# Performance work log

Measured on AMD Instinct MI355X. Metric: run time of the kernel, lower is better.

## Reference

```python
import jax, jax.numpy as jnp
import numpy as np

B, K, N, E, T = 4096, 64, 100000, 128, 3


def setup_inputs() -> dict:
    key = jax.random.key(0)
    ks = jax.random.split(key, 16)
    f = lambda i, shape: jax.random.normal(ks[i], shape, dtype=jnp.float32) * 0.05
    return dict(
        nodes=jax.random.randint(ks[0], (B,), 0, N),
        neigh_idx=jax.random.randint(ks[1], (T, B, K), 0, N),
        node_emb=f(2, (N, E)),
        node_prof=f(3, (N, E)),
        neigh_emb=f(4, (T, N, E)),
        neigh_prof=f(5, (T, N, E)),
        W_f=f(6, (2 * E, E)), b_f=jnp.zeros((E,), jnp.float32),
        Wa1=f(7, (2 * E, E)), ba1=jnp.zeros((E,), jnp.float32),
        Wa2=f(8, (E, E)), ba2=jnp.zeros((E,), jnp.float32),
        Wa3=f(9, (E, 1)), ba3=jnp.zeros((1,), jnp.float32),
        W1=f(10, (E, E)), b1=jnp.zeros((E,), jnp.float32),
        W2=f(11, (E, E)), b2=jnp.zeros((E,), jnp.float32),
        Wc=f(12, (2 * E, E)), bc=jnp.zeros((E,), jnp.float32),
        Wt=f(13, (T * E, T)),
    )


def reference(nodes, neigh_idx, node_emb, node_prof, neigh_emb, neigh_prof,
              W_f, b_f, Wa1, ba1, Wa2, ba2, Wa3, ba3,
              W1, b1, W2, b2, Wc, bc, Wt):
    # fusion(emb, profile) = relu(Linear(concat(emb, profile)))
    fuse = lambda e, p: jax.nn.relu(jnp.concatenate([e, p], -1) @ W_f + b_f)

    nodes_fusion = fuse(node_emb[nodes], node_prof[nodes])            # [B,E]

    per_type = []
    for t in range(T):                                                 # small fixed loop over types
        idx = neigh_idx[t]                                             # [B,K]
        nf = fuse(neigh_emb[t][idx], neigh_prof[t][idx])               # [B,K,E]
        # attention MLP over (neighbor, node) pairs -> softmax over K neighbors
        x = jnp.concatenate(
            [nf, jnp.broadcast_to(nodes_fusion[:, None, :], nf.shape)], -1)  # [B,K,2E]
        h = jax.nn.relu(x @ Wa1 + ba1)
        h = jax.nn.relu(h @ Wa2 + ba2)
        att = jax.nn.softmax((h @ Wa3 + ba3).squeeze(-1), axis=1)      # [B,K]
        agg = jnp.einsum('bke,bk->be', nf, att)                        # weighted neighbor sum
        per_type.append(jax.nn.relu(agg @ W1 + b1))                    # linear_1 + relu

    type_agg = jnp.concatenate(per_type, axis=1)                       # [B,T*E]
    att_t = jax.nn.softmax(type_agg @ Wt, axis=1)                      # [B,T]
    final = jnp.einsum('bte,bt->be', type_agg.reshape(B, T, E), att_t)
    final = jax.nn.relu(final @ W2 + b2)                               # linear_2 + relu
    out = jax.nn.relu(jnp.concatenate([nodes_fusion, final], 1) @ Wc + bc)
    return out, att_t[:, :, None]
```

## Files before the change

kernel.cpp:

```cpp
#include <hip/hip_runtime.h>
#include <hip/hip_bf16.h>

#define B_ 4096
#define K_ 64
#define N_ 100000
#define E_ 128
#define T_ 3

typedef __bf16 bf16x8 __attribute__((ext_vector_type(8)));
typedef float  f32x4  __attribute__((ext_vector_type(4)));

static __device__ __forceinline__ bf16x8 cvt8r(f32x4 u, f32x4 v) {
    bf16x8 o;
    o[0] = (__bf16)u[0]; o[1] = (__bf16)u[1]; o[2] = (__bf16)u[2]; o[3] = (__bf16)u[3];
    o[4] = (__bf16)v[0]; o[5] = (__bf16)v[1]; o[6] = (__bf16)v[2]; o[7] = (__bf16)v[3];
    return o;
}

typedef const __attribute__((address_space(1))) void GAS;
typedef __attribute__((address_space(3))) void LAS;
static __device__ __forceinline__ void gload16(const void* g, void* l) {
    __builtin_amdgcn_global_load_lds((GAS*)g, (LAS*)l, 16, 0, 0);
}

#define MFMA16(a, b, c) __builtin_amdgcn_mfma_f32_16x16x32_bf16((a), (b), (c), 0, 0, 0)

__global__ __launch_bounds__(256)
void k_prep(const float* __restrict__ W_f, const float* __restrict__ Wa1,
            const float* __restrict__ Wa2, const float* __restrict__ W1,
            __bf16* __restrict__ WtF, __bf16* __restrict__ Wa1t,
            __bf16* __restrict__ Wa2t, __bf16* __restrict__ W1t) {
    const int n = blockIdx.x;
    const int k = threadIdx.x;
    if (blockIdx.y == 0) {
        WtF[n * 256 + k] = (__bf16)W_f[k * 128 + n];
    } else if (blockIdx.y == 1) {
        if (k < 128) Wa1t[n * 128 + k] = (__bf16)Wa1[k * 128 + n];
    } else if (blockIdx.y == 2) {
        if (k < 128) Wa2t[n * 128 + k] = (__bf16)Wa2[k * 128 + n];
    } else {
        if (k < 128) W1t[n * 128 + k] = (__bf16)W1[k * 128 + n];
    }
}

__global__ __launch_bounds__(128)
void k_node_fusion(const int* __restrict__ nodes,
                   const float* __restrict__ node_emb,
                   const float* __restrict__ node_prof,
                   const float* __restrict__ W_f, const float* __restrict__ b_f,
                   __bf16* __restrict__ nodes_fusion) {
    __shared__ float x[256];
    const int b = blockIdx.x;
    const int e = threadIdx.x;
    const int nd = nodes[b];
    x[e]       = node_emb[(size_t)nd * E_ + e];
    x[128 + e] = node_prof[(size_t)nd * E_ + e];
    __syncthreads();
    float acc = b_f[e];
#pragma unroll 8
    for (int i = 0; i < 256; ++i) acc = fmaf(x[i], W_f[i * E_ + e], acc);
    nodes_fusion[(size_t)b * E_ + e] = (__bf16)fmaxf(acc, 0.f);
}

__global__ __launch_bounds__(128)
void k_node_pre(const __bf16* __restrict__ nodes_fusion,
                const float* __restrict__ Wa1, const float* __restrict__ ba1,
                float* __restrict__ node_pre) {
    __shared__ float x[128];
    const int b = blockIdx.x;
    const int c = threadIdx.x;
    x[c] = (float)nodes_fusion[(size_t)b * E_ + c];
    __syncthreads();
    float acc = ba1[c];
#pragma unroll 8
    for (int i = 0; i < 128; ++i) acc = fmaf(x[i], Wa1[(128 + i) * E_ + c], acc);
    node_pre[(size_t)b * E_ + c] = acc;
}

#define NF_GRID 1024
#define NF_TPT (N_ / 16)
#define NF_NJOB (NF_TPT * T_)

__global__ __launch_bounds__(256, 4)
void k_nf(const float* __restrict__ neigh_emb,
          const float* __restrict__ neigh_prof,
          const __bf16* __restrict__ WtF, const float* __restrict__ b_f,
          __bf16* __restrict__ NFt) {
    __shared__ __align__(16) float  Xf[2][16 * 256];
    __shared__ __align__(16) __bf16 NFl[16 * 128];

    const int tid  = threadIdx.x;
    const int wid  = tid >> 6, lane = tid & 63;
    const int lr   = lane & 15, lk = lane >> 4;

    bf16x8 wf[16];
#pragma unroll
    for (int ks = 0; ks < 8; ++ks)
#pragma unroll
        for (int n = 0; n < 2; ++n)
            wf[ks * 2 + n] = *(const bf16x8*)&WtF[
                (size_t)(wid * 32 + n * 16 + lr) * 256 + ks * 32 + lk * 8];
    const float bb0 = b_f[wid * 32 + lr];
    const float bb1 = b_f[wid * 32 + 16 + lr];

    auto stage = [&](int j, int buf) {
        const int t    = j / NF_TPT;
        const int base = (j - t * NF_TPT) * 16;
        const float* embT  = neigh_emb  + (size_t)t * N_ * E_;
        const float* profT = neigh_prof + (size_t)t * N_ * E_;
#pragma unroll
        for (int i = 0; i < 4; ++i) {
            const int r  = wid * 4 + i;
            const int id = base + r;
            const int g  = lane ^ (r & 15);
            const float* src = (g < 32)
                ? embT  + (size_t)id * E_ + g * 4
                : profT + (size_t)id * E_ + (g - 32) * 4;
            gload16(src, (char*)&Xf[buf][0] + r * 1024);
        }
    };

    int job = blockIdx.x;
    stage(job, 0);
    int cur = 0;
    bool first = true;

    for (; job < NF_NJOB; job += NF_GRID) {
        const int tc    = job / NF_TPT;
        const int basec = (job - tc * NF_TPT) * 16;

        if (first) { asm volatile("s_waitcnt vmcnt(0)" ::: "memory"); first = false; }
        else       { asm volatile("s_waitcnt vmcnt(1)" ::: "memory"); }
        __builtin_amdgcn_s_barrier();
        __builtin_amdgcn_sched_barrier(0);

        const int nxt = job + NF_GRID;
        if (nxt < NF_NJOB) stage(nxt, cur ^ 1);

        const float* X = &Xf[cur][0];

        {
            f32x4 acc1[2] = {};
#pragma unroll
            for (int ks = 0; ks < 8; ++ks) {
                const int g0 = ks * 8 + lk * 2;
                const f32x4 u0 = *(const f32x4*)&X[lr * 256 + ((g0 ^ lr) << 2)];
                const f32x4 v0 = *(const f32x4*)&X[lr * 256 + (((g0 + 1) ^ lr) << 2)];
                const bf16x8 a0 = cvt8r(u0, v0);
                acc1[0] = MFMA16(a0, wf[ks * 2 + 0], acc1[0]);
                acc1[1] = MFMA16(a0, wf[ks * 2 + 1], acc1[1]);
            }
#pragma unroll
            for (int n = 0; n < 2; ++n) {
                const int c = wid * 32 + n * 16 + lr;
                const float bb = n ? bb1 : bb0;
                const int q = c >> 3, eo = c & 7;
#pragma unroll
                for (int j = 0; j < 4; ++j) {
                    const int rN = lk * 4 + j;
                    NFl[rN * 128 + ((q ^ rN) << 3) + eo] =
                        (__bf16)fmaxf(acc1[n][j] + bb, 0.f);
                }
            }
        }
        asm volatile("s_waitcnt lgkmcnt(0)" ::: "memory");
        __builtin_amdgcn_s_barrier();
        __builtin_amdgcn_sched_barrier(0);

        {
            const int rr = tid >> 4, qq = tid & 15;
            const int p = qq ^ (rr & 15);
            __bf16* outp = NFt + ((size_t)tc * N_ + basec + rr) * E_ + qq * 8;
            *(bf16x8*)outp = *(const bf16x8*)&NFl[rr * 128 + (p << 3)];
        }
        cur ^= 1;
    }
}

__global__ __launch_bounds__(256, 4)
void k_att(const int* __restrict__ neigh_idx,
           const __bf16* __restrict__ NFt,
           const __bf16* __restrict__ Wa1t,
           const __bf16* __restrict__ Wa2t,
           const float* __restrict__ ba2,
           const float* __restrict__ Wa3, const float* __restrict__ ba3,
           const float* __restrict__ node_pre,
           __bf16* __restrict__ aggB) {
    __shared__ __align__(16) __bf16 Nb[64 * 128];
    __shared__ __align__(16) __bf16 H1l[64 * 128];
    __shared__ float npre[128];
    __shared__ float scp[128];
    __shared__ float att_s[64];
    __shared__ float red2[2][128];

    const int b   = blockIdx.x;
    const int t   = blockIdx.y;
    const int tid = threadIdx.x;
    const int wid = tid >> 6, lane = tid & 63;
    const int lr = lane & 15, lk = lane >> 4;

    if (tid < 128) npre[tid] = node_pre[(size_t)b * E_ + tid];

    const int* idx_row = neigh_idx + ((size_t)t * B_ + b) * K_;

#pragma unroll
    for (int i = 0; i < 4; ++i) {
        const int rowblock = wid * 16 + i * 4;
        const int row = rowblock + (lane >> 4);
        const int q = (lane & 15) ^ (row & 15);
        const int id = idx_row[row];
        gload16(NFt + ((size_t)t * N_ + id) * E_ + q * 8,
                (char*)Nb + rowblock * 256);
    }
    __syncthreads();

    {
        f32x4 acc2[4][2] = {};
#pragma unroll
        for (int ks = 0; ks < 4; ++ks) {
            const int q = ks * 4 + lk;
            bf16x8 a[4];
#pragma unroll
            for (int mi = 0; mi < 4; ++mi)
                a[mi] = *(const bf16x8*)&Nb[(mi * 16 + lr) * 128 + ((q ^ lr) << 3)];
#pragma unroll
            for (int n = 0; n < 2; ++n) {
                const bf16x8 w = *(const bf16x8*)&Wa1t[
                    (size_t)(wid * 32 + n * 16 + lr) * 128 + ks * 32 + lk * 8];
#pragma unroll
                for (int mi = 0; mi < 4; ++mi)
                    acc2[mi][n] = MFMA16(a[mi], w, acc2[mi][n]);
            }
        }
#pragma unroll
        for (int n = 0; n < 2; ++n) {
            const int col = wid * 32 + n * 16 + lr;
            const float pp = npre[col];
            const int q = col >> 3, eo = col & 7;
#pragma unroll
            for (int mi = 0; mi < 4; ++mi)
#pragma unroll
                for (int j = 0; j < 4; ++j) {
                    const int row = mi * 16 + lk * 4 + j;
                    H1l[row * 128 + ((q ^ (row & 15)) << 3) + eo] =
                        (__bf16)fmaxf(acc2[mi][n][j] + pp, 0.f);
                }
        }
    }
    __syncthreads();

    const int mp = wid >> 1, h = wid & 1;
    const int r0 = 32 * mp + lr, r1 = r0 + 16;
    {
        f32x4 acc[2][4] = {};
#pragma unroll
        for (int ks = 0; ks < 4; ++ks) {
            const int q = ks * 4 + lk;
            const bf16x8 a0 = *(const bf16x8*)&H1l[r0 * 128 + ((q ^ lr) << 3)];
            const bf16x8 a1 = *(const bf16x8*)&H1l[r1 * 128 + ((q ^ lr) << 3)];
            const __bf16* wb = Wa2t + (size_t)(h * 64 + lr) * 128 + ks * 32 + lk * 8;
#pragma unroll
            for (int n = 0; n < 4; ++n) {
                const bf16x8 w = *(const bf16x8*)(wb + (size_t)n * 16 * 128);
                acc[0][n] = MFMA16(a0, w, acc[0][n]);
                acc[1][n] = MFMA16(a1, w, acc[1][n]);
            }
        }
        float ba2r[4], wa3r[4];
#pragma unroll
        for (int n = 0; n < 4; ++n) {
            const int col = h * 64 + n * 16 + lr;
            ba2r[n] = ba2[col];
            wa3r[n] = Wa3[col];
        }
#pragma unroll
        for (int mi = 0; mi < 2; ++mi)
#pragma unroll
            for (int j = 0; j < 4; ++j) {
                float v = 0.f;
#pragma unroll
                for (int n = 0; n < 4; ++n)
                    v += fmaxf(acc[mi][n][j] + ba2r[n], 0.f) * wa3r[n];
                v += __shfl_xor(v, 1);
                v += __shfl_xor(v, 2);
                v += __shfl_xor(v, 4);
                v += __shfl_xor(v, 8);
                if (lr == 0)
                    scp[h * 64 + 32 * mp + mi * 16 + lk * 4 + j] = v;
            }
    }
    __syncthreads();

    if (tid < 64) {
        const float v = scp[tid] + scp[64 + tid] + ba3[0];
        float m = v;
#pragma unroll
        for (int o = 32; o > 0; o >>= 1) m = fmaxf(m, __shfl_xor(m, o));
        const float pe = __expf(v - m);
        float s = pe;
#pragma unroll
        for (int o = 32; o > 0; o >>= 1) s += __shfl_xor(s, o);
        att_s[tid] = pe / s;
    }
    __syncthreads();

    {
        const int e = tid & 127, half = tid >> 7;
        const int q = e >> 3, eo = e & 7;
        float a = 0.f;
#pragma unroll 8
        for (int n = 0; n < 32; ++n) {
            const int nn = half * 32 + n;
            a = fmaf(att_s[nn], (float)Nb[nn * 128 + ((q ^ (nn & 15)) << 3) + eo], a);
        }
        red2[half][e] = a;
    }
    __syncthreads();
    if (tid < 128) {
        aggB[((size_t)b * T_ + t) * E_ + tid] = (__bf16)(red2[0][tid] + red2[1][tid]);
    }
}

__global__ __launch_bounds__(256)
void k_w1(const __bf16* __restrict__ aggB, const __bf16* __restrict__ W1t,
          const float* __restrict__ b1, __bf16* __restrict__ type_agg) {
    const int tid  = threadIdx.x;
    const int wid  = tid >> 6;
    const int lane = tid & 63;
    const int lr   = lane & 15;
    const int lk   = lane >> 4;
    const int rbase = blockIdx.x * 64 + wid * 16;

    f32x4 acc[8] = {};
#pragma unroll
    for (int ks = 0; ks < 4; ++ks) {
        const bf16x8 a = *(const bf16x8*)&aggB[(size_t)(rbase + lr) * 128 + ks * 32 + lk * 8];
        const __bf16* wb = W1t + (size_t)lr * 128 + ks * 32 + lk * 8;
#pragma unroll
        for (int n = 0; n < 8; ++n) {
            const bf16x8 w = *(const bf16x8*)(wb + (size_t)n * 16 * 128);
            acc[n] = MFMA16(a, w, acc[n]);
        }
    }
#pragma unroll
    for (int n = 0; n < 8; ++n) {
        const int col = n * 16 + lr;
        const float bb = b1[col];
#pragma unroll
        for (int j = 0; j < 4; ++j) {
            const int row = rbase + lk * 4 + j;
            type_agg[(size_t)row * 128 + col] = (__bf16)fmaxf(acc[n][j] + bb, 0.f);
        }
    }
}

__global__ __launch_bounds__(128)
void k_final(const __bf16* __restrict__ type_agg,
             const __bf16* __restrict__ nodes_fusion,
             const float* __restrict__ Wt,
             const float* __restrict__ W2, const float* __restrict__ b2,
             const float* __restrict__ Wc, const float* __restrict__ bc,
             float* __restrict__ out, float* __restrict__ att_out) {
    __shared__ float ta[384];
    __shared__ float nfu[128];
    __shared__ float fin[128];
    __shared__ float hb[128];
    __shared__ float att[3];
    __shared__ float red[3][128];

    const int b = blockIdx.x;
    const int e = threadIdx.x;

    const float v0 = (float)type_agg[(size_t)b * 384 + e];
    const float v1 = (float)type_agg[(size_t)b * 384 + 128 + e];
    const float v2 = (float)type_agg[(size_t)b * 384 + 256 + e];
    ta[e] = v0; ta[128 + e] = v1; ta[256 + e] = v2;
    nfu[e] = (float)nodes_fusion[(size_t)b * E_ + e];

    float p0, p1, p2;
    {
        const float* w0 = Wt + (size_t)e * 3;
        const float* w1 = Wt + (size_t)(128 + e) * 3;
        const float* w2 = Wt + (size_t)(256 + e) * 3;
        p0 = v0 * w0[0] + v1 * w1[0] + v2 * w2[0];
        p1 = v0 * w0[1] + v1 * w1[1] + v2 * w2[1];
        p2 = v0 * w0[2] + v1 * w1[2] + v2 * w2[2];
    }
    red[0][e] = p0; red[1][e] = p1; red[2][e] = p2;
    __syncthreads();

    if (e < 3) {
        float s = 0.f;
        for (int i = 0; i < 128; ++i) s += red[e][i];
        red[e][0] = s;
    }
    __syncthreads();
    if (e == 0) {
        const float s0 = red[0][0], s1 = red[1][0], s2 = red[2][0];
        const float m  = fmaxf(s0, fmaxf(s1, s2));
        const float e0 = __expf(s0 - m), e1 = __expf(s1 - m), e2 = __expf(s2 - m);
        const float inv = 1.f / (e0 + e1 + e2);
        att[0] = e0 * inv; att[1] = e1 * inv; att[2] = e2 * inv;
    }
    __syncthreads();

    fin[e] = att[0] * ta[e] + att[1] * ta[128 + e] + att[2] * ta[256 + e];
    __syncthreads();

    float acc = b2[e];
#pragma unroll 8
    for (int i = 0; i < 128; ++i) acc = fmaf(fin[i], W2[i * E_ + e], acc);
    hb[e] = fmaxf(acc, 0.f);
    __syncthreads();

    float acc2 = bc[e];
#pragma unroll 8
    for (int i = 0; i < 128; ++i) acc2 = fmaf(nfu[i], Wc[i * E_ + e], acc2);
#pragma unroll 8
    for (int i = 0; i < 128; ++i) acc2 = fmaf(hb[i], Wc[(128 + i) * E_ + e], acc2);
    out[(size_t)b * E_ + e] = fmaxf(acc2, 0.f);

    if (e < 3) att_out[(size_t)b * 3 + e] = att[e];
}

extern "C" void kernel_launch(void* const* d_in, const int* in_sizes, int n_in,
                              void* d_out, int out_size, void* d_ws, size_t ws_size,
                              hipStream_t stream) {
    const int*   nodes      = (const int*)d_in[0];
    const int*   neigh_idx  = (const int*)d_in[1];
    const float* node_emb   = (const float*)d_in[2];
    const float* node_prof  = (const float*)d_in[3];
    const float* neigh_emb  = (const float*)d_in[4];
    const float* neigh_prof = (const float*)d_in[5];
    const float* W_f = (const float*)d_in[6];  const float* b_f = (const float*)d_in[7];
    const float* Wa1 = (const float*)d_in[8];  const float* ba1 = (const float*)d_in[9];
    const float* Wa2 = (const float*)d_in[10]; const float* ba2 = (const float*)d_in[11];
    const float* Wa3 = (const float*)d_in[12]; const float* ba3 = (const float*)d_in[13];
    const float* W1  = (const float*)d_in[14]; const float* b1  = (const float*)d_in[15];
    const float* W2  = (const float*)d_in[16]; const float* b2  = (const float*)d_in[17];
    const float* Wc  = (const float*)d_in[18]; const float* bc  = (const float*)d_in[19];
    const float* Wt  = (const float*)d_in[20];

    float* out     = (float*)d_out;
    float* att_out = out + (size_t)B_ * E_;

    char* ws = (char*)d_ws;
    __bf16* nodes_fusion = (__bf16*)(ws);
    float*  node_pre     = (float*)(ws + (1u << 20));
    __bf16* type_agg     = (__bf16*)(ws + (3u << 20));
    __bf16* aggB         = (__bf16*)(ws + (6u << 20));
    __bf16* WtF          = (__bf16*)(ws + (9u << 20));
    __bf16* Wa1t         = (__bf16*)(ws + (9u << 20) + 65536);
    __bf16* Wa2t         = (__bf16*)(ws + (9u << 20) + 98304);
    __bf16* W1t          = (__bf16*)(ws + (9u << 20) + 131072);
    __bf16* NFt          = (__bf16*)(ws + (16u << 20));

    k_prep<<<dim3(128, 4), 256, 0, stream>>>(W_f, Wa1, Wa2, W1, WtF, Wa1t, Wa2t, W1t);
    k_node_fusion<<<B_, 128, 0, stream>>>(nodes, node_emb, node_prof, W_f, b_f,
                                          nodes_fusion);
    k_node_pre<<<B_, 128, 0, stream>>>(nodes_fusion, Wa1, ba1, node_pre);
    k_nf<<<NF_GRID, 256, 0, stream>>>(neigh_emb, neigh_prof, WtF, b_f, NFt);
    k_att<<<dim3(B_, T_), 256, 0, stream>>>(neigh_idx, NFt, Wa1t, Wa2t, ba2,
                                            Wa3, ba3, node_pre, aggB);
    k_w1<<<(B_ * T_) / 64, 256, 0, stream>>>(aggB, W1t, b1, type_agg);
    k_final<<<B_, 128, 0, stream>>>(type_agg, nodes_fusion, Wt, W2, b2, Wc, bc,
                                    out, att_out);
}
```

Before: 315.2 us.

## Make attention kernel persistent with double-buffered neighbor gather and register-resident weights

Turns k_att into a persistent kernel of 768 blocks, each looping over 16 (b,t) jobs. While the current job computes, the next job's neighbor-row gather is issued into a second LDS buffer. Wa1/Wa2 weight fragments are held in registers instead of being reloaded from global memory for every job. The second GEMM is re-split so each wave owns 32 output columns, and the weighted sum is reduced across four waves. This trades occupancy (launch bounds 4→3, two LDS buffers) for hiding gather latency and removing per-block weight reloads and launch overhead.

```diff
diff --git a/kernel.cpp b/kernel.cpp
--- a/kernel.cpp
+++ b/kernel.cpp
@@ -177,7 +177,11 @@
     }
 }
 
-__global__ __launch_bounds__(256, 4)
+#define ATT_GRID 768
+#define ATT_NJOB (B_ * T_)
+#define ATT_NITER (ATT_NJOB / ATT_GRID)
+
+__global__ __launch_bounds__(256, 3)
 void k_att(const int* __restrict__ neigh_idx,
            const __bf16* __restrict__ NFt,
            const __bf16* __restrict__ Wa1t,
@@ -186,138 +190,182 @@
            const float* __restrict__ Wa3, const float* __restrict__ ba3,
            const float* __restrict__ node_pre,
            __bf16* __restrict__ aggB) {
-    __shared__ __align__(16) __bf16 Nb[64 * 128];
+    __shared__ __align__(16) __bf16 Nb[2][64 * 128];
     __shared__ __align__(16) __bf16 H1l[64 * 128];
-    __shared__ float npre[128];
-    __shared__ float scp[128];
-    __shared__ float att_s[64];
-    __shared__ float red2[2][128];
-
-    const int b   = blockIdx.x;
-    const int t   = blockIdx.y;
+    __shared__ float scp[4 * 64];
+    __shared__ float red4[4 * 128];
+
     const int tid = threadIdx.x;
     const int wid = tid >> 6, lane = tid & 63;
     const int lr = lane & 15, lk = lane >> 4;
 
-    if (tid < 128) npre[tid] = node_pre[(size_t)b * E_ + tid];
-
-    const int* idx_row = neigh_idx + ((size_t)t * B_ + b) * K_;
-
-#pragma unroll
-    for (int i = 0; i < 4; ++i) {
-        const int rowblock = wid * 16 + i * 4;
-        const int row = rowblock + (lane >> 4);
-        const int q = (lane & 15) ^ (row & 15);
-        const int id = idx_row[row];
-        gload16(NFt + ((size_t)t * N_ + id) * E_ + q * 8,
-                (char*)Nb + rowblock * 256);
-    }
-    __syncthreads();
-
+    bf16x8 wa1r[8], wa2r[8];
+#pragma unroll
+    for (int ks = 0; ks < 4; ++ks)
+#pragma unroll
+        for (int n = 0; n < 2; ++n) {
+            wa1r[ks * 2 + n] = *(const bf16x8*)&Wa1t[
+                (size_t)(wid * 32 + n * 16 + lr) * 128 + ks * 32 + lk * 8];
+            wa2r[ks * 2 + n] = *(const bf16x8*)&Wa2t[
+                (size_t)(wid * 32 + n * 16 + lr) * 128 + ks * 32 + lk * 8];
+        }
+    float ba2r[2], wa3r[2];
+#pragma unroll
+    for (int n = 0; n < 2; ++n) {
+        ba2r[n] = ba2[wid * 32 + n * 16 + lr];
+        wa3r[n] = Wa3[wid * 32 + n * 16 + lr];
+    }
+    const float ba3v = ba3[0];
+
+    auto stage = [&](int j, int buf, int idv) {
+        const int t = j / B_;
+        const __bf16* tab = NFt + (size_t)t * N_ * E_;
+#pragma unroll
+        for (int i = 0; i < 4; ++i) {
+            const int rowblock = wid * 16 + i * 4;
+            const int rsub = i * 4 + (lane >> 4);
+            const int q = (lane & 15) ^ rsub;
+            const int id = __shfl(idv, rsub);
+            gload16(tab + (size_t)id * E_ + q * 8,
+                    (char*)&Nb[buf][0] + rowblock * 256);
+        }
+    };
+
+    int job = blockIdx.x;
     {
-        f32x4 acc2[4][2] = {};
-#pragma unroll
-        for (int ks = 0; ks < 4; ++ks) {
-            const int q = ks * 4 + lk;
-            bf16x8 a[4];
+        const int idv0 = neigh_idx[(size_t)job * K_ + wid * 16 + (lane & 15)];
+        stage(job, 0, idv0);
+    }
+    float npn0 = node_pre[(size_t)(job % B_) * E_ + wid * 32 + lr];
+    float npn1 = node_pre[(size_t)(job % B_) * E_ + wid * 32 + 16 + lr];
+    int jn = job + ATT_GRID; if (jn >= ATT_NJOB) jn = ATT_NJOB - 1;
+    int idnext = neigh_idx[(size_t)jn * K_ + wid * 16 + (lane & 15)];
+    int cur = 0;
+
+    for (int it = 0; it < ATT_NITER; ++it, job += ATT_GRID) {
+        asm volatile("s_waitcnt vmcnt(0)" ::: "memory");
+        __builtin_amdgcn_s_barrier();
+        __builtin_amdgcn_sched_barrier(0);
+
+        const float np0 = npn0, np1 = npn1;
+
+        if (it + 1 < ATT_NITER) {
+            stage(job + ATT_GRID, cur ^ 1, idnext);
+            int j2 = job + 2 * ATT_GRID; if (j2 >= ATT_NJOB) j2 = ATT_NJOB - 1;
+            idnext = neigh_idx[(size_t)j2 * K_ + wid * 16 + (lane & 15)];
+            const int bn = (job + ATT_GRID) % B_;
+            npn0 = node_pre[(size_t)bn * E_ + wid * 32 + lr];
+            npn1 = node_pre[(size_t)bn * E_ + wid * 32 + 16 + lr];
+        }
+
+        const __bf16* NbC = &Nb[cur][0];
+
+        {
+            f32x4 acc2[4][2] = {};
+#pragma unroll
+            for (int ks = 0; ks < 4; ++ks) {
+                const int q = ks * 4 + lk;
+                bf16x8 a[4];
+#pragma unroll
+                for (int mi = 0; mi < 4; ++mi)
+                    a[mi] = *(const bf16x8*)&NbC[(mi * 16 + lr) * 128 + ((q ^ lr) << 3)];
+#pragma unroll
+                for (int n = 0; n < 2; ++n)
+#pragma unroll
+                    for (int mi = 0; mi < 4; ++mi)
+                        acc2[mi][n] = MFMA16(a[mi], wa1r[ks * 2 + n], acc2[mi][n]);
+            }
+#pragma unroll
+            for (int n = 0; n < 2; ++n) {
+                const int col = wid * 32 + n * 16 + lr;
+                const float pp = n ? np1 : np0;
+                const int q = col >> 3, eo = col & 7;
+#pragma unroll
+                for (int mi = 0; mi < 4; ++mi)
+#pragma unroll
+                    for (int j = 0; j < 4; ++j) {
+                        const int row = mi * 16 + lk * 4 + j;
+                        H1l[row * 128 + ((q ^ (row & 15)) << 3) + eo] =
+                            (__bf16)fmaxf(acc2[mi][n][j] + pp, 0.f);
+                    }
+            }
+        }
+        asm volatile("s_waitcnt lgkmcnt(0)" ::: "memory");
+        __builtin_amdgcn_s_barrier();
+        __builtin_amdgcn_sched_barrier(0);
+
+        {
+            f32x4 acc3[4][2] = {};
+#pragma unroll
+            for (int ks = 0; ks < 4; ++ks) {
+                const int q = ks * 4 + lk;
+                bf16x8 a[4];
+#pragma unroll
+                for (int mi = 0; mi < 4; ++mi)
+                    a[mi] = *(const bf16x8*)&H1l[(mi * 16 + lr) * 128 + ((q ^ lr) << 3)];
+#pragma unroll
+                for (int n = 0; n < 2; ++n)
+#pragma unroll
+                    for (int mi = 0; mi < 4; ++mi)
+                        acc3[mi][n] = MFMA16(a[mi], wa2r[ks * 2 + n], acc3[mi][n]);
+            }
 #pragma unroll
             for (int mi = 0; mi < 4; ++mi)
-                a[mi] = *(const bf16x8*)&Nb[(mi * 16 + lr) * 128 + ((q ^ lr) << 3)];
-#pragma unroll
-            for (int n = 0; n < 2; ++n) {
-                const bf16x8 w = *(const bf16x8*)&Wa1t[
-                    (size_t)(wid * 32 + n * 16 + lr) * 128 + ks * 32 + lk * 8];
-#pragma unroll
-                for (int mi = 0; mi < 4; ++mi)
-                    acc2[mi][n] = MFMA16(a[mi], w, acc2[mi][n]);
+#pragma unroll
+                for (int j = 0; j < 4; ++j) {
+                    float v = fmaxf(acc3[mi][0][j] + ba2r[0], 0.f) * wa3r[0]
+                            + fmaxf(acc3[mi][1][j] + ba2r[1], 0.f) * wa3r[1];
+                    v += __shfl_xor(v, 1);
+                    v += __shfl_xor(v, 2);
+                    v += __shfl_xor(v, 4);
+                    v += __shfl_xor(v, 8);
+                    if (lr == 0)
+                        scp[wid * 64 + mi * 16 + lk * 4 + j] = v;
+                }
+        }
+        asm volatile("s_waitcnt lgkmcnt(0)" ::: "memory");
+        __builtin_amdgcn_s_barrier();
+        __builtin_amdgcn_sched_barrier(0);
+
+        float att;
+        {
+            const float v = scp[lane] + scp[64 + lane] + scp[128 + lane]
+                          + scp[192 + lane] + ba3v;
+            float m = v;
+#pragma unroll
+            for (int o = 32; o > 0; o >>= 1) m = fmaxf(m, __shfl_xor(m, o));
+            const float pe = __expf(v - m);
+            float s = pe;
+#pragma unroll
+            for (int o = 32; o > 0; o >>= 1) s += __shfl_xor(s, o);
+            att = pe / s;
+        }
+
+        {
+            float p0 = 0.f, p1 = 0.f;
+            const int q0 = lane >> 3, eo = lane & 7;
+            const int q1 = (lane + 64) >> 3;
+#pragma unroll
+            for (int i = 0; i < 16; ++i) {
+                const int row = wid * 16 + i;
+                const float av = __shfl(att, row);
+                p0 = fmaf(av, (float)NbC[row * 128 + ((q0 ^ (row & 15)) << 3) + eo], p0);
+                p1 = fmaf(av, (float)NbC[row * 128 + ((q1 ^ (row & 15)) << 3) + eo], p1);
             }
-        }
-#pragma unroll
-        for (int n = 0; n < 2; ++n) {
-            const int col = wid * 32 + n * 16 + lr;
-            const float pp = npre[col];
-            const int q = col >> 3, eo = col & 7;
-#pragma unroll
-            for (int mi = 0; mi < 4; ++mi)
-#pragma unroll
-                for (int j = 0; j < 4; ++j) {
-                    const int row = mi * 16 + lk * 4 + j;
-                    H1l[row * 128 + ((q ^ (row & 15)) << 3) + eo] =
-                        (__bf16)fmaxf(acc2[mi][n][j] + pp, 0.f);
-                }
-        }
-    }
-    __syncthreads();
-
-    const int mp = wid >> 1, h = wid & 1;
-    const int r0 = 32 * mp + lr, r1 = r0 + 16;
-    {
-        f32x4 acc[2][4] = {};
-#pragma unroll
-        for (int ks = 0; ks < 4; ++ks) {
-            const int q = ks * 4 + lk;
-            const bf16x8 a0 = *(const bf16x8*)&H1l[r0 * 128 + ((q ^ lr) << 3)];
-            const bf16x8 a1 = *(const bf16x8*)&H1l[r1 * 128 + ((q ^ lr) << 3)];
-            const __bf16* wb = Wa2t + (size_t)(h * 64 + lr) * 128 + ks * 32 + lk * 8;
-#pragma unroll
-            for (int n = 0; n < 4; ++n) {
-                const bf16x8 w = *(const bf16x8*)(wb + (size_t)n * 16 * 128);
-                acc[0][n] = MFMA16(a0, w, acc[0][n]);
-                acc[1][n] = MFMA16(a1, w, acc[1][n]);
-            }
-        }
-        float ba2r[4], wa3r[4];
-#pragma unroll
-        for (int n = 0; n < 4; ++n) {
-            const int col = h * 64 + n * 16 + lr;
-            ba2r[n] = ba2[col];
-            wa3r[n] = Wa3[col];
-        }
-#pragma unroll
-        for (int mi = 0; mi < 2; ++mi)
-#pragma unroll
-            for (int j = 0; j < 4; ++j) {
-                float v = 0.f;
-#pragma unroll
-                for (int n = 0; n < 4; ++n)
-                    v += fmaxf(acc[mi][n][j] + ba2r[n], 0.f) * wa3r[n];
-                v += __shfl_xor(v, 1);
-                v += __shfl_xor(v, 2);
-                v += __shfl_xor(v, 4);
-                v += __shfl_xor(v, 8);
-                if (lr == 0)
-                    scp[h * 64 + 32 * mp + mi * 16 + lk * 4 + j] = v;
-            }
-    }
-    __syncthreads();
-
-    if (tid < 64) {
-        const float v = scp[tid] + scp[64 + tid] + ba3[0];
-        float m = v;
-#pragma unroll
-        for (int o = 32; o > 0; o >>= 1) m = fmaxf(m, __shfl_xor(m, o));
-        const float pe = __expf(v - m);
-        float s = pe;
-#pragma unroll
-        for (int o = 32; o > 0; o >>= 1) s += __shfl_xor(s, o);
-        att_s[tid] = pe / s;
-    }
-    __syncthreads();
-
-    {
-        const int e = tid & 127, half = tid >> 7;
-        const int q = e >> 3, eo = e & 7;
-        float a = 0.f;
-#pragma unroll 8
-        for (int n = 0; n < 32; ++n) {
-            const int nn = half * 32 + n;
-            a = fmaf(att_s[nn], (float)Nb[nn * 128 + ((q ^ (nn & 15)) << 3) + eo], a);
-        }
-        red2[half][e] = a;
-    }
-    __syncthreads();
-    if (tid < 128) {
-        aggB[((size_t)b * T_ + t) * E_ + tid] = (__bf16)(red2[0][tid] + red2[1][tid]);
+            red4[wid * 128 + lane] = p0;
+            red4[wid * 128 + 64 + lane] = p1;
+        }
+        asm volatile("s_waitcnt lgkmcnt(0)" ::: "memory");
+        __builtin_amdgcn_s_barrier();
+        __builtin_amdgcn_sched_barrier(0);
+
+        if (tid < 128) {
+            const float s = red4[tid] + red4[128 + tid] + red4[256 + tid]
+                          + red4[384 + tid];
+            const int bcur = job % B_, tcur = job / B_;
+            aggB[((size_t)bcur * T_ + tcur) * E_ + tid] = (__bf16)s;
+        }
+        cur ^= 1;
     }
 }
 
@@ -460,8 +508,8 @@
                                           nodes_fusion);
     k_node_pre<<<B_, 128, 0, stream>>>(nodes_fusion, Wa1, ba1, node_pre);
     k_nf<<<NF_GRID, 256, 0, stream>>>(neigh_emb, neigh_prof, WtF, b_f, NFt);
-    k_att<<<dim3(B_, T_), 256, 0, stream>>>(neigh_idx, NFt, Wa1t, Wa2t, ba2,
-                                            Wa3, ba3, node_pre, aggB);
+    k_att<<<ATT_GRID, 256, 0, stream>>>(neigh_idx, NFt, Wa1t, Wa2t, ba2,
+                                        Wa3, ba3, node_pre, aggB);
     k_w1<<<(B_ * T_) / 64, 256, 0, stream>>>(aggB, W1t, b1, type_agg);
     k_final<<<B_, 128, 0, stream>>>(type_agg, nodes_fusion, Wt, W2, b2, Wc, bc,
                                     out, att_out);
```

New measurement: 420.3 us. 1.33x slower.
